# Kernel optimization log

Measured on AMD Instinct MI355X. Metric: run time of the kernel, lower is better.

The kernel has to match this reference:

```python
import jax, jax.numpy as jnp
import numpy as np

N_S = 4096      # number of sentences
N_K = 8192      # number of knowledge entries
HID = 1024      # settings.hidden_dim
SENT = 1024     # settings.sent_dim


def setup_inputs() -> dict:
    key = jax.random.key(0)
    ks = jax.random.split(key, 6)
    sentences = jax.random.normal(ks[0], (N_S, SENT), dtype=jnp.float32)
    knowledge = jax.random.normal(ks[1], (N_K, 3 * HID), dtype=jnp.float32)
    # Linear params stored as [in, out] for x @ W + b
    Ws = jax.random.normal(ks[2], (SENT, HID), dtype=jnp.float32) * 0.02
    bs = jnp.zeros((HID,), dtype=jnp.float32)
    Wk = jax.random.normal(ks[3], (3 * HID, HID), dtype=jnp.float32) * 0.02
    bk = jnp.zeros((HID,), dtype=jnp.float32)
    return {"sentences": sentences, "knowledge": knowledge,
            "Ws": Ws, "bs": bs, "Wk": Wk, "bk": bk}


def reference(sentences, knowledge, Ws, bs, Wk, bk):
    S = sentences @ Ws + bs                  # [N_s, h]
    K = knowledge @ Wk + bk                  # [N_k, h]
    align_scores = S @ K.T                   # [N_s, N_k]
    # NOTE: softmax over dim=0 (sentence axis), exactly as the torch module
    attentions = jax.nn.softmax(align_scores, axis=0)
    fused = attentions @ knowledge           # [N_s, 3h]
    return (fused, attentions)
```

## Files before the change

### kernel.cpp

```cpp
#include <hip/hip_runtime.h>
#include <hip/hip_bf16.h>
#include <cstdint>
#include <cstddef>

#define N_S 4096
#define N_Kn 8192
#define HID 1024
#define SENT 1024
#define K3 3072

typedef __attribute__((ext_vector_type(4))) float f4;
typedef __attribute__((ext_vector_type(8))) short bf8;
typedef __attribute__((ext_vector_type(4))) short bf4;
typedef unsigned short u16;

__device__ __forceinline__ u16 f2bf(float x) {
    __hip_bfloat16 h = __float2bfloat16(x);
    return __builtin_bit_cast(u16, h);
}
__device__ __forceinline__ float bf2f(u16 u) {
    union { unsigned int u; float f; } v; v.u = ((unsigned int)u) << 16;
    return v.f;
}

__device__ __forceinline__ void gl16(const u16* g, u16* l) {
    __builtin_amdgcn_global_load_lds(
        (const __attribute__((address_space(1))) void*)g,
        (__attribute__((address_space(3))) void*)l, 16, 0, 0);
}

__device__ __forceinline__ int xcd_swz(int bid, int nwg) {
    const int cpx = nwg >> 3;
    return (bid & 7) * cpx + (bid >> 3);
}

#define BARR __builtin_amdgcn_s_barrier()
#define PRIO1 __builtin_amdgcn_s_setprio(1)
#define PRIO0 __builtin_amdgcn_s_setprio(0)
#define VM8  asm volatile("s_waitcnt vmcnt(8)" ::: "memory")
#define VM7  asm volatile("s_waitcnt vmcnt(7)" ::: "memory")
#define VM6  asm volatile("s_waitcnt vmcnt(6)" ::: "memory")
#define VM2  asm volatile("s_waitcnt vmcnt(2)" ::: "memory")
#define VM0  asm volatile("s_waitcnt vmcnt(0)" ::: "memory")
#define LGKM0 asm volatile("s_waitcnt lgkmcnt(0)" ::: "memory")

__global__ __launch_bounds__(256) void transpose_split_f32(
    const float* __restrict__ in, u16* __restrict__ hi, u16* __restrict__ lo,
    int R, int C)
{
    __shared__ float tile[32][33];
    const int bx = blockIdx.x * 32, by = blockIdx.y * 32;
    const int tx = threadIdx.x & 31, ty = threadIdx.x >> 5;
#pragma unroll
    for (int i = 0; i < 32; i += 8)
        tile[ty + i][tx] = in[(size_t)(by + ty + i) * C + bx + tx];
    __syncthreads();
#pragma unroll
    for (int i = 0; i < 32; i += 8) {
        const float v = tile[tx][ty + i];
        const u16 h = f2bf(v);
        const size_t o = (size_t)(bx + ty + i) * R + by + tx;
        hi[o] = h;
        lo[o] = f2bf(v - bf2f(h));
    }
}

__global__ __launch_bounds__(256) void transpose_f32_bf16(
    const float* __restrict__ in, u16* __restrict__ out, int R, int C)
{
    __shared__ float tile[32][33];
    const int bx = blockIdx.x * 32, by = blockIdx.y * 32;
    const int tx = threadIdx.x & 31, ty = threadIdx.x >> 5;
#pragma unroll
    for (int i = 0; i < 32; i += 8)
        tile[ty + i][tx] = in[(size_t)(by + ty + i) * C + bx + tx];
    __syncthreads();
#pragma unroll
    for (int i = 0; i < 32; i += 8)
        out[(size_t)(bx + ty + i) * R + by + tx] = f2bf(tile[tx][ty + i]);
}

#define GB_LDA(buf, mh) \
  _Pragma("unroll") for (int mf_ = 0; mf_ < 2; ++mf_) \
  _Pragma("unroll") for (int kk_ = 0; kk_ < 2; ++kk_) \
    fa[mf_][kk_] = *(const bf8*)&sA[buf][(wm*64 + ((mh)*2+mf_)*16 + fr)*64 + (((kk_*4+kg) ^ (fr&7))<<3)];

#define GB_LDB(buf, nh, FB) \
  _Pragma("unroll") for (int nf_ = 0; nf_ < 3; ++nf_) \
  _Pragma("unroll") for (int kk_ = 0; kk_ < 2; ++kk_) \
    FB[nf_][kk_] = *(const bf8*)&sB[buf][(wn*96 + ((nh)*3+nf_)*16 + fr)*64 + (((kk_*4+kg) ^ (fr&7))<<3)];

#define GB_MMA(mh, nh, FB) \
  _Pragma("unroll") for (int kk_ = 0; kk_ < 2; ++kk_) \
  _Pragma("unroll") for (int mf_ = 0; mf_ < 2; ++mf_) \
  _Pragma("unroll") for (int nf_ = 0; nf_ < 3; ++nf_) \
    acc[(mh)*2+mf_][(nh)*3+nf_] = __builtin_amdgcn_mfma_f32_16x16x32_bf16( \
        fa[mf_][kk_], FB[nf_][kk_], acc[(mh)*2+mf_][(nh)*3+nf_], 0, 0, 0);

__global__ __launch_bounds__(512, 2) void gemm8b(
    const u16* __restrict__ A, const u16* __restrict__ B,
    float* __restrict__ C, int N, int Kd, int gx)
{
    __shared__ u16 sA[2][256 * 64];
    __shared__ u16 sB[2][192 * 64];

    const int swz = xcd_swz(blockIdx.x, gridDim.x);
    const int bx = swz % gx, by = swz / gx;
    const long brow = (long)by * 256, bcol = (long)bx * 192;

    const int t = threadIdx.x;
    const int w = t >> 6, l = t & 63;
    const int fr = l & 15, kg = l >> 4;
    const int wm = w >> 1;
    const int wn = w & 1;

    const int srow = t >> 3;
    const int schk = ((t & 7) ^ (srow & 7)) << 3;
    const int sldb = w << 9;

    const u16* pA0 = A + (brow +   0 + srow) * (long)Kd + schk;
    const u16* pA1 = A + (brow +  64 + srow) * (long)Kd + schk;
    const u16* pA2 = A + (brow + 128 + srow) * (long)Kd + schk;
    const u16* pA3 = A + (brow + 192 + srow) * (long)Kd + schk;
    const u16* pB0 = B + (bcol +   0 + srow) * (long)Kd + schk;
    const u16* pB1 = B + (bcol +  64 + srow) * (long)Kd + schk;
    const u16* pB2 = B + (bcol + 128 + srow) * (long)Kd + schk;

    auto stB3 = [&](int buf) {
        u16* base = &sB[buf][0];
        gl16(pB0, base + sldb);
        gl16(pB1, base + 4096 + sldb);
        gl16(pB2, base + 8192 + sldb);
    };
    auto stA4 = [&](int buf) {
        u16* base = &sA[buf][0];
        gl16(pA0, base + sldb);
        gl16(pA1, base + 4096 + sldb);
        gl16(pA2, base + 8192 + sldb);
        gl16(pA3, base + 12288 + sldb);
    };
    auto advance = [&]() {
        pA0 += 64; pA1 += 64; pA2 += 64; pA3 += 64;
        pB0 += 64; pB1 += 64; pB2 += 64;
    };

    f4 acc[4][6];
#pragma unroll
    for (int m = 0; m < 4; ++m)
#pragma unroll
        for (int n = 0; n < 6; ++n) acc[m][n] = (f4){0.f, 0.f, 0.f, 0.f};

    bf8 fa[2][2], fb0[3][2], fb1[3][2];

    const int NK = Kd >> 6;

    stB3(0); stA4(0); advance();
    stB3(1); stA4(1); advance();
    VM7;
    BARR;
    GB_LDB(0, 0, fb0);

    for (int kt = 0; kt < NK; ++kt) {
        const int buf = kt & 1;
        const bool s2 = kt + 2 < NK;
        const bool more = kt + 1 < NK;

        GB_LDA(buf, 0);
        BARR; PRIO1; GB_MMA(0, 0, fb0); PRIO0;

        GB_LDB(buf, 1, fb1);
        BARR; PRIO1; GB_MMA(0, 1, fb1); PRIO0;

        GB_LDA(buf, 1);
        if (s2) { stB3(buf); }
        BARR; PRIO1; GB_MMA(1, 0, fb0); PRIO0;

        if (s2) { stA4(buf); VM7; } else { VM0; }
        BARR;
        if (more) { GB_LDB(buf ^ 1, 0, fb0); }
        PRIO1; GB_MMA(1, 1, fb1); PRIO0;
        advance();
    }

#pragma unroll
    for (int n = 0; n < 6; ++n) {
        const long c = bcol + wn * 96 + n * 16 + fr;
#pragma unroll
        for (int m = 0; m < 4; ++m) {
            const long r0 = brow + wm * 64 + m * 16 + kg * 4;
#pragma unroll
            for (int r = 0; r < 4; ++r)
                C[(r0 + r) * (long)N + c] = acc[m][n][r];
        }
    }
}

#define GS_LD(buf) \
  _Pragma("unroll") for (int m_ = 0; m_ < 4; ++m_) { \
    fah[m_] = *(const bf8*)&sAh[buf][(wm*64 + m_*16 + fr)*32 + kq]; \
    fal[m_] = *(const bf8*)&sAl[buf][(wm*64 + m_*16 + fr)*32 + kq]; } \
  _Pragma("unroll") for (int j_ = 0; j_ < 4; ++j_) { \
    fbh[j_] = *(const bf8*)&sBh[buf][(wn*64 + j_*16 + fr)*32 + kq]; \
    fbl[j_] = *(const bf8*)&sBl[buf][(wn*64 + j_*16 + fr)*32 + kq]; }

#define GS_MMA(nlo) \
  _Pragma("unroll") for (int m_ = 0; m_ < 4; ++m_) \
  _Pragma("unroll") for (int j_ = 0; j_ < 2; ++j_) { \
    const int n_ = (nlo)*2 + j_; \
    acc[m_][n_] = __builtin_amdgcn_mfma_f32_16x16x32_bf16(fah[m_], fbh[n_], acc[m_][n_], 0, 0, 0); \
    acc[m_][n_] = __builtin_amdgcn_mfma_f32_16x16x32_bf16(fah[m_], fbl[n_], acc[m_][n_], 0, 0, 0); \
    acc[m_][n_] = __builtin_amdgcn_mfma_f32_16x16x32_bf16(fal[m_], fbh[n_], acc[m_][n_], 0, 0, 0); }

__global__ __launch_bounds__(512, 2) void gemm8s(
    const u16* __restrict__ Ah, const u16* __restrict__ Al,
    const u16* __restrict__ Bh, const u16* __restrict__ Bl,
    float* __restrict__ C, float* __restrict__ pm, float* __restrict__ ps,
    int N, int Kd)
{
    __shared__ u16 sAh[2][8192], sAl[2][8192];
    __shared__ u16 sBh[2][4096], sBl[2][4096];

    const int bid = blockIdx.x;
    const int q = bid >> 3;
    const int by = (bid & 7) * 2 + (q & 1);
    const int bx = q >> 1;
    const long brow = (long)by * 256, bcol = (long)bx * 128;

    const int t = threadIdx.x;
    const int w = t >> 6, l = t & 63;
    const int fr = l & 15, kg = l >> 4;
    const int wm = w >> 1;
    const int wn = w & 1;
    const int kq = (kg ^ ((fr >> 1) & 3)) << 3;

    const int srow = t >> 2;
    const int schk = ((t & 3) ^ ((t >> 3) & 3)) << 3;
    const int sldb = w << 9;

    const u16* pAh0 = Ah + (brow + srow) * (long)Kd + schk;
    const u16* pAh1 = Ah + (brow + 128 + srow) * (long)Kd + schk;
    const u16* pAl0 = Al + (brow + srow) * (long)Kd + schk;
    const u16* pAl1 = Al + (brow + 128 + srow) * (long)Kd + schk;
    const u16* pBh0 = Bh + (bcol + srow) * (long)Kd + schk;
    const u16* pBl0 = Bl + (bcol + srow) * (long)Kd + schk;

    auto stage6 = [&](int buf) {
        gl16(pBh0, &sBh[buf][sldb]);
        gl16(pBl0, &sBl[buf][sldb]);
        gl16(pAh0, &sAh[buf][sldb]);
        gl16(pAh1, &sAh[buf][4096 + sldb]);
        gl16(pAl0, &sAl[buf][sldb]);
        gl16(pAl1, &sAl[buf][4096 + sldb]);
    };
    auto advance = [&]() {
        pAh0 += 32; pAh1 += 32; pAl0 += 32; pAl1 += 32;
        pBh0 += 32; pBl0 += 32;
    };

    f4 acc[4][4];
#pragma unroll
    for (int m = 0; m < 4; ++m)
#pragma unroll
        for (int n = 0; n < 4; ++n) acc[m][n] = (f4){0.f, 0.f, 0.f, 0.f};

    bf8 fah[4], fal[4], fbh[4], fbl[4];

    const int NK = Kd >> 5;

    stage6(0); advance();
    stage6(1); advance();
    VM6;
    BARR;

    for (int kt = 0; kt < NK; ++kt) {
        const int buf = kt & 1;
        const bool s2 = kt + 2 < NK;

        GS_LD(buf);
        BARR; PRIO1; GS_MMA(0); PRIO0;

        if (s2) { stage6(buf); VM6; } else { VM0; }
        BARR;
        PRIO1; GS_MMA(1); PRIO0;
        advance();
    }

#pragma unroll
    for (int n = 0; n < 4; ++n) {
        const long c = bcol + wn * 64 + n * 16 + fr;
#pragma unroll
        for (int m = 0; m < 4; ++m) {
            const long r0 = brow + wm * 64 + m * 16 + kg * 4;
#pragma unroll
            for (int r = 0; r < 4; ++r)
                C[(r0 + r) * (long)N + c] = acc[m][n][r];
        }
    }

    float* red = (float*)&sAh[0][0];
    float lmax[4];
#pragma unroll
    for (int n = 0; n < 4; ++n) {
        float m = -3.4e38f;
#pragma unroll
        for (int mm = 0; mm < 4; ++mm)
#pragma unroll
            for (int r = 0; r < 4; ++r) m = fmaxf(m, acc[mm][n][r]);
        m = fmaxf(m, __shfl_xor(m, 16, 64));
        m = fmaxf(m, __shfl_xor(m, 32, 64));
        lmax[n] = m;
    }
    BARR;
    if (kg == 0) {
#pragma unroll
        for (int n = 0; n < 4; ++n)
            red[wm * 128 + wn * 64 + n * 16 + fr] = lmax[n];
    }
    BARR;
    float bmax[4];
#pragma unroll
    for (int n = 0; n < 4; ++n) {
        const int c = wn * 64 + n * 16 + fr;
        bmax[n] = fmaxf(fmaxf(red[c], red[128 + c]),
                        fmaxf(red[256 + c], red[384 + c]));
    }
    BARR;
    float lsum[4];
#pragma unroll
    for (int n = 0; n < 4; ++n) {
        float s = 0.f;
#pragma unroll
        for (int mm = 0; mm < 4; ++mm)
#pragma unroll
            for (int r = 0; r < 4; ++r) s += __expf(acc[mm][n][r] - bmax[n]);
        s += __shfl_xor(s, 16, 64);
        s += __shfl_xor(s, 32, 64);
        lsum[n] = s;
    }
    if (kg == 0) {
#pragma unroll
        for (int n = 0; n < 4; ++n)
            red[wm * 128 + wn * 64 + n * 16 + fr] = lsum[n];
    }
    BARR;
    if (wm == 0 && kg == 0) {
#pragma unroll
        for (int n = 0; n < 4; ++n) {
            const int c = wn * 64 + n * 16 + fr;
            const float bs = red[c] + red[128 + c] + red[256 + c] + red[384 + c];
            pm[(size_t)by * N + bcol + c] = bmax[n];
            ps[(size_t)by * N + bcol + c] = bs;
        }
    }
}

__global__ __launch_bounds__(512, 2) void gemm8f(
    const float* __restrict__ Af, const u16* __restrict__ Bh, const u16* __restrict__ Bl,
    u16* __restrict__ Chi, u16* __restrict__ Clo, const float* __restrict__ bias,
    int N, int Kd)
{
    __shared__ u16 sAh[2][8192], sAl[2][8192];
    __shared__ u16 sBh[2][4096], sBl[2][4096];

    const int bid = blockIdx.x;
    const int q = bid >> 3;
    const int by = ((bid & 7) << 2) | (q & 3);
    const int bx = q >> 2;
    const long brow = (long)by * 256, bcol = (long)bx * 128;

    const int t = threadIdx.x;
    const int w = t >> 6, l = t & 63;
    const int fr = l & 15, kg = l >> 4;
    const int wm = w >> 1;
    const int wn = w & 1;
    const int kq = (kg ^ ((fr >> 1) & 3)) << 3;

    const int srow = t >> 2;
    const int schk = ((t & 3) ^ ((t >> 3) & 3)) << 3;
    const int sldb = w << 9;
    const u16* pBh0 = Bh + (bcol + srow) * (long)Kd + schk;
    const u16* pBl0 = Bl + (bcol + srow) * (long)Kd + schk;

    const float* pA0 = Af + (brow + srow) * (long)Kd + (t & 3) * 8;
    const float* pA1 = Af + (brow + 128 + srow) * (long)Kd + (t & 3) * 8;
    const int adst = srow * 32 + schk;

    auto cvt_write = [&](int buf, int dst, const f4& x0, const f4& x1) {
        float xv[8];
        *(f4*)&xv[0] = x0; *(f4*)&xv[4] = x1;
        u16 h[8], lw[8];
#pragma unroll
        for (int j = 0; j < 8; ++j) {
            h[j] = f2bf(xv[j]);
            lw[j] = f2bf(xv[j] - bf2f(h[j]));
        }
        *(bf8*)&sAh[buf][dst] = *(bf8*)h;
        *(bf8*)&sAl[buf][dst] = *(bf8*)lw;
    };

    f4 acc[4][4];
#pragma unroll
    for (int m = 0; m < 4; ++m)
#pragma unroll
        for (int n = 0; n < 4; ++n) acc[m][n] = (f4){0.f, 0.f, 0.f, 0.f};

    bf8 fah[4], fal[4], fbh[4], fbl[4];

    const int NK = Kd >> 5;

    {
        f4 a00 = *(const f4*)(pA0);      f4 a01 = *(const f4*)(pA0 + 4);
        f4 a10 = *(const f4*)(pA1);      f4 a11 = *(const f4*)(pA1 + 4);
        gl16(pBh0, &sBh[0][sldb]); gl16(pBl0, &sBl[0][sldb]);
        f4 b00 = *(const f4*)(pA0 + 32); f4 b01 = *(const f4*)(pA0 + 36);
        f4 b10 = *(const f4*)(pA1 + 32); f4 b11 = *(const f4*)(pA1 + 36);
        gl16(pBh0 + 32, &sBh[1][sldb]); gl16(pBl0 + 32, &sBl[1][sldb]);
        VM8;
        cvt_write(0, adst, a00, a01);
        cvt_write(0, adst + 4096, a10, a11);
        VM2;
        cvt_write(1, adst, b00, b01);
        cvt_write(1, adst + 4096, b10, b11);
        LGKM0;
        BARR;
        pA0 += 64; pA1 += 64; pBh0 += 64; pBl0 += 64;
    }

    for (int kt = 0; kt < NK; ++kt) {
        const int buf = kt & 1;
        const bool s2 = kt + 2 < NK;

        GS_LD(buf);
        f4 x0, x1, y0, y1;
        if (s2) {
            x0 = *(const f4*)(pA0); x1 = *(const f4*)(pA0 + 4);
            y0 = *(const f4*)(pA1); y1 = *(const f4*)(pA1 + 4);
        }
        BARR; PRIO1; GS_MMA(0); PRIO0;

        if (s2) {
            gl16(pBh0, &sBh[buf][sldb]);
            gl16(pBl0, &sBl[buf][sldb]);
            VM2;
            cvt_write(buf, adst, x0, x1);
            cvt_write(buf, adst + 4096, y0, y1);
            LGKM0;
        } else {
            VM0;
        }
        BARR;
        PRIO1; GS_MMA(1); PRIO0;
        pA0 += 32; pA1 += 32; pBh0 += 32; pBl0 += 32;
    }

#pragma unroll
    for (int n = 0; n < 4; ++n) {
        const long c = bcol + wn * 64 + n * 16 + fr;
        const float bv = bias[c];
#pragma unroll
        for (int m = 0; m < 4; ++m) {
            const long r0 = brow + wm * 64 + m * 16 + kg * 4;
#pragma unroll
            for (int r = 0; r < 4; ++r) {
                const float v = acc[m][n][r] + bv;
                const u16 h = f2bf(v);
                Chi[(r0 + r) * (long)N + c] = h;
                Clo[(r0 + r) * (long)N + c] = f2bf(v - bf2f(h));
            }
        }
    }
}

template <bool SPLIT, bool AF32, bool EPIS>
__global__ __launch_bounds__(256) void gemm_mfma(
    const void* __restrict__ Aany, const u16* __restrict__ Alo_,
    const u16* __restrict__ Bhi_, const u16* __restrict__ Blo_,
    float* __restrict__ Cf, u16* __restrict__ Chi, u16* __restrict__ Clo,
    const float* __restrict__ bias, int N, int Kd, int gx)
{
    constexpr int SA = AF32 ? 48 : 32;
    __shared__ u16 sAh[128 * SA];
    __shared__ u16 sAl[SPLIT ? 128 * SA : 8];
    __shared__ u16 sBh[128 * 32];
    __shared__ u16 sBl[SPLIT ? 128 * 32 : 8];

    const int swz = xcd_swz(blockIdx.x, gridDim.x);
    const int nst_x = gx >> 2;
    const int st = swz >> 4, off = swz & 15;
    const int bxi = (st % nst_x) * 4 + (off & 3);
    const int byi = (st / nst_x) * 4 + (off >> 2);

    const int t = threadIdx.x;
    const int w = t >> 6;
    const int l = t & 63;
    const long brow = (long)byi * 128;
    const long bcol = (long)bxi * 128;

    const int grow = l >> 2;
    const int gcol = ((l & 3) ^ ((l >> 3) & 3)) * 8;

    const int wr = (w >> 1) * 64;
    const int wc = (w & 1) * 64;
    const int fr = l & 15;
    const int kg = l >> 4;
    const int kq = (kg ^ ((fr >> 1) & 3)) * 8;

    f4 acc[4][4];
#pragma unroll
    for (int m = 0; m < 4; m++)
#pragma unroll
        for (int n = 0; n < 4; n++) acc[m][n] = (f4){0.f, 0.f, 0.f, 0.f};

    const int nkt = Kd >> 5;
    for (int kt = 0; kt < nkt; ++kt) {
        const int k0 = kt * 32;

#pragma unroll
        for (int i = 0; i < 2; ++i) {
            const long r = bcol + i * 64 + w * 16 + grow;
            const int lb = i * 2048 + w * 512;
            gl16(Bhi_ + r * Kd + k0 + gcol, sBh + lb);
            if constexpr (SPLIT) gl16(Blo_ + r * Kd + k0 + gcol, sBl + lb);
        }

        if constexpr (!AF32) {
            const u16* Ahi = (const u16*)Aany;
#pragma unroll
            for (int i = 0; i < 2; ++i) {
                const long r = brow + i * 64 + w * 16 + grow;
                const int lb = i * 2048 + w * 512;
                gl16(Ahi + r * Kd + k0 + gcol, sAh + lb);
                if constexpr (SPLIT) gl16(Alo_ + r * Kd + k0 + gcol, sAl + lb);
            }
        } else {
            const float* Af = (const float*)Aany;
            const int ar = w * 8 + (l >> 3);
            const int cF = (l & 7) * 4;
#pragma unroll
            for (int j = 0; j < 4; ++j) {
                const int r = j * 32 + ar;
                const f4 v = *(const f4*)(Af + (brow + r) * (long)Kd + k0 + cF);
                u16 h[4], lw[4];
#pragma unroll
                for (int qq = 0; qq < 4; ++qq) {
                    h[qq] = f2bf(v[qq]);
                    if constexpr (SPLIT) lw[qq] = f2bf(v[qq] - bf2f(h[qq]));
                }
                *(bf4*)&sAh[r * SA + cF] = *(bf4*)h;
                if constexpr (SPLIT) *(bf4*)&sAl[r * SA + cF] = *(bf4*)lw;
            }
        }
        __syncthreads();

        bf8 fah[4], fbh[4], fal[4], fbl[4];
#pragma unroll
        for (int m = 0; m < 4; ++m) {
            if constexpr (AF32) {
                fah[m] = *(bf8*)&sAh[(wr + m * 16 + fr) * SA + kg * 8];
                if constexpr (SPLIT) fal[m] = *(bf8*)&sAl[(wr + m * 16 + fr) * SA + kg * 8];
            } else {
                fah[m] = *(bf8*)&sAh[(wr + m * 16 + fr) * 32 + kq];
                if constexpr (SPLIT) fal[m] = *(bf8*)&sAl[(wr + m * 16 + fr) * 32 + kq];
            }
            fbh[m] = *(bf8*)&sBh[(wc + m * 16 + fr) * 32 + kq];
            if constexpr (SPLIT) fbl[m] = *(bf8*)&sBl[(wc + m * 16 + fr) * 32 + kq];
        }
#pragma unroll
        for (int m = 0; m < 4; ++m)
#pragma unroll
            for (int n = 0; n < 4; ++n) {
                acc[m][n] = __builtin_amdgcn_mfma_f32_16x16x32_bf16(fah[m], fbh[n], acc[m][n], 0, 0, 0);
                if constexpr (SPLIT) {
                    acc[m][n] = __builtin_amdgcn_mfma_f32_16x16x32_bf16(fah[m], fbl[n], acc[m][n], 0, 0, 0);
                    acc[m][n] = __builtin_amdgcn_mfma_f32_16x16x32_bf16(fal[m], fbh[n], acc[m][n], 0, 0, 0);
                }
            }
        __syncthreads();
    }

#pragma unroll
    for (int n = 0; n < 4; ++n) {
        const long c = bcol + wc + n * 16 + fr;
        float bv = 0.f;
        if constexpr (EPIS) bv = bias[c];
#pragma unroll
        for (int m = 0; m < 4; ++m) {
            const long r0 = brow + wr + m * 16 + kg * 4;
#pragma unroll
            for (int r = 0; r < 4; ++r) {
                const float v = acc[m][n][r] + bv;
                if constexpr (EPIS) {
                    const u16 h = f2bf(v);
                    Chi[(r0 + r) * (long)N + c] = h;
                    Clo[(r0 + r) * (long)N + c] = f2bf(v - bf2f(h));
                } else {
                    Cf[(r0 + r) * (long)N + c] = v;
                }
            }
        }
    }
}

#define RCHUNK 128

__global__ __launch_bounds__(256) void softmax_combine(
    const float* __restrict__ pm, const float* __restrict__ ps,
    float* __restrict__ fm, float* __restrict__ fsinv)
{
    const int col = blockIdx.x * 256 + threadIdx.x;
    float m = -3.4e38f;
#pragma unroll
    for (int i = 0; i < 16; i++) m = fmaxf(m, pm[(size_t)i * N_Kn + col]);
    float s = 0.f;
#pragma unroll
    for (int i = 0; i < 16; i++)
        s += ps[(size_t)i * N_Kn + col] * __expf(pm[(size_t)i * N_Kn + col] - m);
    fm[col] = m;
    fsinv[col] = 1.f / s;
}

__global__ __launch_bounds__(256) void softmax_norm(
    float* __restrict__ align, u16* __restrict__ abf,
    const float* __restrict__ fm, const float* __restrict__ fsinv)
{
    const int col = blockIdx.x * 256 + threadIdx.x;
    const int r0 = blockIdx.y * RCHUNK;
    const float m = fm[col], si = fsinv[col];
    for (int r = 0; r < RCHUNK; r++) {
        const size_t idx = (size_t)(r0 + r) * N_Kn + col;
        const float v = __expf(align[idx] - m) * si;
        align[idx] = v;
        abf[idx] = f2bf(v);
    }
}

extern "C" void kernel_launch(void* const* d_in, const int* in_sizes, int n_in,
                              void* d_out, int out_size, void* d_ws, size_t ws_size,
                              hipStream_t stream)
{
    const float* sentences = (const float*)d_in[0];
    const float* knowledge = (const float*)d_in[1];
    const float* Ws = (const float*)d_in[2];
    const float* bs = (const float*)d_in[3];
    const float* Wk = (const float*)d_in[4];
    const float* bk = (const float*)d_in[5];

    float* out_fused = (float*)d_out;
    float* out_attn = (float*)d_out + (size_t)N_S * K3;

    char* w = (char*)d_ws;
    u16* attn_bf = (u16*)w;
    u16* WsT_hi = (u16*)w; w += (size_t)HID * SENT * 2;
    u16* WsT_lo = (u16*)w; w += (size_t)HID * SENT * 2;
    u16* WkT_hi = (u16*)w; w += (size_t)HID * K3 * 2;
    u16* WkT_lo = (u16*)w; w += (size_t)HID * K3 * 2;
    u16* S_hi   = (u16*)w; w += (size_t)N_S * HID * 2;
    u16* S_lo   = (u16*)w; w += (size_t)N_S * HID * 2;
    u16* K_hi   = (u16*)w; w += (size_t)N_Kn * HID * 2;
    u16* K_lo   = (u16*)w; w += (size_t)N_Kn * HID * 2;
    u16* kT     = (u16*)w; w += (size_t)K3 * N_Kn * 2;
    float* pm   = (float*)w; w += (size_t)16 * N_Kn * 4;
    float* ps   = (float*)w; w += (size_t)16 * N_Kn * 4;
    float* fm   = (float*)w; w += (size_t)N_Kn * 4;
    float* fsv  = (float*)w; w += (size_t)N_Kn * 4;

    transpose_split_f32<<<dim3(HID / 32, SENT / 32), 256, 0, stream>>>(Ws, WsT_hi, WsT_lo, SENT, HID);
    transpose_split_f32<<<dim3(HID / 32, K3 / 32), 256, 0, stream>>>(Wk, WkT_hi, WkT_lo, K3, HID);
    transpose_f32_bf16<<<dim3(K3 / 32, N_Kn / 32), 256, 0, stream>>>(knowledge, kT, N_Kn, K3);

    gemm_mfma<true, true, true><<<(HID / 128) * (N_S / 128), 256, 0, stream>>>(
        sentences, nullptr, WsT_hi, WsT_lo, nullptr, S_hi, S_lo, bs, HID, SENT, HID / 128);

    gemm8f<<<256, 512, 0, stream>>>(
        knowledge, WkT_hi, WkT_lo, K_hi, K_lo, bk, HID, K3);

    gemm8s<<<(N_Kn / 128) * (N_S / 256), 512, 0, stream>>>(
        S_hi, S_lo, K_hi, K_lo, out_attn, pm, ps, N_Kn, HID);

    softmax_combine<<<dim3(N_Kn / 256), 256, 0, stream>>>(pm, ps, fm, fsv);
    softmax_norm<<<dim3(N_Kn / 256, N_S / RCHUNK), 256, 0, stream>>>(out_attn, attn_bf, fm, fsv);

    gemm8b<<<(K3 / 192) * (N_S / 256), 512, 0, stream>>>(
        attn_bf, kT, out_fused, K3, N_Kn, K3 / 192);
}
```

Baseline: 679.5 us.

## Reuse gemm8f for sentence projection, vectorize softmax_norm, merge MMA barrier in gemm8b

The generic gemm_mfma kernel for the sentence projection is replaced with the gemm8f kernel, which gains a parameter for block-index swizzling so it can handle the smaller 4096-row problem with 128 blocks. softmax_norm now handles two columns per thread using float2 loads and stores and packed bf16 writes, halving its grid. In the 192-wide gemm loop, two MFMA groups are merged under one barrier to remove a sync. With only 128 blocks, the sentence GEMM may underfill the GPU's compute units.

After: 676.6 us (median of 2 runs). About the same (-0.4%).

```diff
diff --git a/kernel.cpp b/kernel.cpp
--- a/kernel.cpp
+++ b/kernel.cpp
@@ -166,10 +166,8 @@
         const bool more = kt + 1 < NK;
 
         GB_LDA(buf, 0);
-        BARR; PRIO1; GB_MMA(0, 0, fb0); PRIO0;
-
         GB_LDB(buf, 1, fb1);
-        BARR; PRIO1; GB_MMA(0, 1, fb1); PRIO0;
+        BARR; PRIO1; GB_MMA(0, 0, fb0); GB_MMA(0, 1, fb1); PRIO0;
 
         GB_LDA(buf, 1);
         if (s2) { stB3(buf); }
@@ -357,15 +355,15 @@
 __global__ __launch_bounds__(512, 2) void gemm8f(
     const float* __restrict__ Af, const u16* __restrict__ Bh, const u16* __restrict__ Bl,
     u16* __restrict__ Chi, u16* __restrict__ Clo, const float* __restrict__ bias,
-    int N, int Kd)
+    int N, int Kd, int lsh)
 {
     __shared__ u16 sAh[2][8192], sAl[2][8192];
     __shared__ u16 sBh[2][4096], sBl[2][4096];
 
     const int bid = blockIdx.x;
     const int q = bid >> 3;
-    const int by = ((bid & 7) << 2) | (q & 3);
-    const int bx = q >> 2;
+    const int by = ((bid & 7) << lsh) | (q & ((1 << lsh) - 1));
+    const int bx = q >> lsh;
     const long brow = (long)by * 256, bcol = (long)bx * 128;
 
     const int t = threadIdx.x;
@@ -471,136 +469,6 @@
     }
 }
 
-template <bool SPLIT, bool AF32, bool EPIS>
-__global__ __launch_bounds__(256) void gemm_mfma(
-    const void* __restrict__ Aany, const u16* __restrict__ Alo_,
-    const u16* __restrict__ Bhi_, const u16* __restrict__ Blo_,
-    float* __restrict__ Cf, u16* __restrict__ Chi, u16* __restrict__ Clo,
-    const float* __restrict__ bias, int N, int Kd, int gx)
-{
-    constexpr int SA = AF32 ? 48 : 32;
-    __shared__ u16 sAh[128 * SA];
-    __shared__ u16 sAl[SPLIT ? 128 * SA : 8];
-    __shared__ u16 sBh[128 * 32];
-    __shared__ u16 sBl[SPLIT ? 128 * 32 : 8];
-
-    const int swz = xcd_swz(blockIdx.x, gridDim.x);
-    const int nst_x = gx >> 2;
-    const int st = swz >> 4, off = swz & 15;
-    const int bxi = (st % nst_x) * 4 + (off & 3);
-    const int byi = (st / nst_x) * 4 + (off >> 2);
-
-    const int t = threadIdx.x;
-    const int w = t >> 6;
-    const int l = t & 63;
-    const long brow = (long)byi * 128;
-    const long bcol = (long)bxi * 128;
-
-    const int grow = l >> 2;
-    const int gcol = ((l & 3) ^ ((l >> 3) & 3)) * 8;
-
-    const int wr = (w >> 1) * 64;
-    const int wc = (w & 1) * 64;
-    const int fr = l & 15;
-    const int kg = l >> 4;
-    const int kq = (kg ^ ((fr >> 1) & 3)) * 8;
-
-    f4 acc[4][4];
-#pragma unroll
-    for (int m = 0; m < 4; m++)
-#pragma unroll
-        for (int n = 0; n < 4; n++) acc[m][n] = (f4){0.f, 0.f, 0.f, 0.f};
-
-    const int nkt = Kd >> 5;
-    for (int kt = 0; kt < nkt; ++kt) {
-        const int k0 = kt * 32;
-
-#pragma unroll
-        for (int i = 0; i < 2; ++i) {
-            const long r = bcol + i * 64 + w * 16 + grow;
-            const int lb = i * 2048 + w * 512;
-            gl16(Bhi_ + r * Kd + k0 + gcol, sBh + lb);
-            if constexpr (SPLIT) gl16(Blo_ + r * Kd + k0 + gcol, sBl + lb);
-        }
-
-        if constexpr (!AF32) {
-            const u16* Ahi = (const u16*)Aany;
-#pragma unroll
-            for (int i = 0; i < 2; ++i) {
-                const long r = brow + i * 64 + w * 16 + grow;
-                const int lb = i * 2048 + w * 512;
-                gl16(Ahi + r * Kd + k0 + gcol, sAh + lb);
-                if constexpr (SPLIT) gl16(Alo_ + r * Kd + k0 + gcol, sAl + lb);
-            }
-        } else {
-            const float* Af = (const float*)Aany;
-            const int ar = w * 8 + (l >> 3);
-            const int cF = (l & 7) * 4;
-#pragma unroll
-            for (int j = 0; j < 4; ++j) {
-                const int r = j * 32 + ar;
-                const f4 v = *(const f4*)(Af + (brow + r) * (long)Kd + k0 + cF);
-                u16 h[4], lw[4];
-#pragma unroll
-                for (int qq = 0; qq < 4; ++qq) {
-                    h[qq] = f2bf(v[qq]);
-                    if constexpr (SPLIT) lw[qq] = f2bf(v[qq] - bf2f(h[qq]));
-                }
-                *(bf4*)&sAh[r * SA + cF] = *(bf4*)h;
-                if constexpr (SPLIT) *(bf4*)&sAl[r * SA + cF] = *(bf4*)lw;
-            }
-        }
-        __syncthreads();
-
-        bf8 fah[4], fbh[4], fal[4], fbl[4];
-#pragma unroll
-        for (int m = 0; m < 4; ++m) {
-            if constexpr (AF32) {
-                fah[m] = *(bf8*)&sAh[(wr + m * 16 + fr) * SA + kg * 8];
-                if constexpr (SPLIT) fal[m] = *(bf8*)&sAl[(wr + m * 16 + fr) * SA + kg * 8];
-            } else {
-                fah[m] = *(bf8*)&sAh[(wr + m * 16 + fr) * 32 + kq];
-                if constexpr (SPLIT) fal[m] = *(bf8*)&sAl[(wr + m * 16 + fr) * 32 + kq];
-            }
-            fbh[m] = *(bf8*)&sBh[(wc + m * 16 + fr) * 32 + kq];
-            if constexpr (SPLIT) fbl[m] = *(bf8*)&sBl[(wc + m * 16 + fr) * 32 + kq];
-        }
-#pragma unroll
-        for (int m = 0; m < 4; ++m)
-#pragma unroll
-            for (int n = 0; n < 4; ++n) {
-                acc[m][n] = __builtin_amdgcn_mfma_f32_16x16x32_bf16(fah[m], fbh[n], acc[m][n], 0, 0, 0);
-                if constexpr (SPLIT) {
-                    acc[m][n] = __builtin_amdgcn_mfma_f32_16x16x32_bf16(fah[m], fbl[n], acc[m][n], 0, 0, 0);
-                    acc[m][n] = __builtin_amdgcn_mfma_f32_16x16x32_bf16(fal[m], fbh[n], acc[m][n], 0, 0, 0);
-                }
-            }
-        __syncthreads();
-    }
-
-#pragma unroll
-    for (int n = 0; n < 4; ++n) {
-        const long c = bcol + wc + n * 16 + fr;
-        float bv = 0.f;
-        if constexpr (EPIS) bv = bias[c];
-#pragma unroll
-        for (int m = 0; m < 4; ++m) {
-            const long r0 = brow + wr + m * 16 + kg * 4;
-#pragma unroll
-            for (int r = 0; r < 4; ++r) {
-                const float v = acc[m][n][r] + bv;
-                if constexpr (EPIS) {
-                    const u16 h = f2bf(v);
-                    Chi[(r0 + r) * (long)N + c] = h;
-                    Clo[(r0 + r) * (long)N + c] = f2bf(v - bf2f(h));
-                } else {
-                    Cf[(r0 + r) * (long)N + c] = v;
-                }
-            }
-        }
-    }
-}
-
 #define RCHUNK 128
 
 __global__ __launch_bounds__(256) void softmax_combine(
@@ -623,14 +491,18 @@
     float* __restrict__ align, u16* __restrict__ abf,
     const float* __restrict__ fm, const float* __restrict__ fsinv)
 {
-    const int col = blockIdx.x * 256 + threadIdx.x;
+    const int col = (blockIdx.x * 256 + threadIdx.x) * 2;
     const int r0 = blockIdx.y * RCHUNK;
-    const float m = fm[col], si = fsinv[col];
+    const float m0 = fm[col], m1 = fm[col + 1];
+    const float s0 = fsinv[col], s1 = fsinv[col + 1];
     for (int r = 0; r < RCHUNK; r++) {
         const size_t idx = (size_t)(r0 + r) * N_Kn + col;
-        const float v = __expf(align[idx] - m) * si;
-        align[idx] = v;
-        abf[idx] = f2bf(v);
+        const float2 x = *(const float2*)&align[idx];
+        const float v0 = __expf(x.x - m0) * s0;
+        const float v1 = __expf(x.y - m1) * s1;
+        *(float2*)&align[idx] = make_float2(v0, v1);
+        const unsigned int p = (unsigned int)f2bf(v0) | ((unsigned int)f2bf(v1) << 16);
+        *(unsigned int*)&abf[idx] = p;
     }
 }
 
@@ -668,17 +540,17 @@
     transpose_split_f32<<<dim3(HID / 32, K3 / 32), 256, 0, stream>>>(Wk, WkT_hi, WkT_lo, K3, HID);
     transpose_f32_bf16<<<dim3(K3 / 32, N_Kn / 32), 256, 0, stream>>>(knowledge, kT, N_Kn, K3);
 
-    gemm_mfma<true, true, true><<<(HID / 128) * (N_S / 128), 256, 0, stream>>>(
-        sentences, nullptr, WsT_hi, WsT_lo, nullptr, S_hi, S_lo, bs, HID, SENT, HID / 128);
+    gemm8f<<<128, 512, 0, stream>>>(
+        sentences, WsT_hi, WsT_lo, S_hi, S_lo, bs, HID, SENT, 1);
 
     gemm8f<<<256, 512, 0, stream>>>(
-        knowledge, WkT_hi, WkT_lo, K_hi, K_lo, bk, HID, K3);
+        knowledge, WkT_hi, WkT_lo, K_hi, K_lo, bk, HID, K3, 2);
 
     gemm8s<<<(N_Kn / 128) * (N_S / 256), 512, 0, stream>>>(
         S_hi, S_lo, K_hi, K_lo, out_attn, pm, ps, N_Kn, HID);
 
     softmax_combine<<<dim3(N_Kn / 256), 256, 0, stream>>>(pm, ps, fm, fsv);
-    softmax_norm<<<dim3(N_Kn / 256, N_S / RCHUNK), 256, 0, stream>>>(out_attn, attn_bf, fm, fsv);
+    softmax_norm<<<dim3(N_Kn / 512, N_S / RCHUNK), 256, 0, stream>>>(out_attn, attn_bf, fm, fsv);
 
     gemm8b<<<(K3 / 192) * (N_S / 256), 512, 0, stream>>>(
         attn_bf, kT, out_fused, K3, N_Kn, K3 / 192);
```
